# Optimization experiments

Hardware: AMD Instinct MI355X
Metric: run time of the kernel (lower is better)

Reference implementation:

```python
import jax, jax.numpy as jnp
import numpy as np

B, D, U = 4096, 2048, 2048

def hard_sigmoid(x):
    # keras hard_sigmoid: clip(0.2*x + 0.5, 0, 1)
    return jnp.clip(0.2 * x + 0.5, 0.0, 1.0)

def setup_inputs() -> dict:
    key = jax.random.key(0)
    k1, k2, k3, k4, k5 = jax.random.split(key, 5)
    return {
        "inputs": jax.random.normal(k1, (B, D), dtype=jnp.float32),
        "h_tm1": jax.random.normal(k2, (B, U), dtype=jnp.float32),
        "c_tm1": jax.random.normal(k3, (B, U), dtype=jnp.float32),
        "kernel": jax.random.normal(k4, (D, 4 * U), dtype=jnp.float32) * 0.02,
        "recurrent_kernel": jax.random.normal(k5, (U, 4 * U), dtype=jnp.float32) * 0.02,
    }

def reference(inputs, h_tm1, c_tm1, kernel, recurrent_kernel):
    u = kernel.shape[1] // 4
    # One fused GEMM each for input and recurrent paths (same math as 8 split GEMMs)
    z = inputs @ kernel + h_tm1 @ recurrent_kernel  # [B, 4U]
    z_i, z_f, z_c, z_o = jnp.split(z, 4, axis=1)
    i = hard_sigmoid(z_i)
    f = hard_sigmoid(z_f)
    c = f * c_tm1 + i * jnp.tanh(z_c)
    o = hard_sigmoid(z_o)
    h = o * jnp.tanh(c)
    return (h, h, c)
```

## Files before the change

### kernel.cpp

```cpp
#include <hip/hip_runtime.h>
#include <stdint.h>

typedef unsigned short u16;
typedef float f32x4 __attribute__((ext_vector_type(4)));
typedef __bf16 bf16x8 __attribute__((ext_vector_type(8)));

#define B_ 4096
#define D_ 2048
#define U_ 2048
#define K_ 4096
#define N_ 8192
#define NIT 32

__device__ __forceinline__ u16 f32_bf16(float f) {
  uint32_t u = __float_as_uint(f);
  u += 0x7FFFu + ((u >> 16) & 1u);
  return (u16)(u >> 16);
}
__device__ __forceinline__ float hsig(float x) {
  return fminf(fmaxf(0.2f * x + 0.5f, 0.0f), 1.0f);
}
__device__ __forceinline__ float ftanh(float x) {
  x = fminf(fmaxf(x, -15.0f), 15.0f);
  float e = __expf(2.0f * x);
  return (e - 1.0f) / (e + 1.0f);
}
__device__ __forceinline__ void gload16(const void* g, void* l) {
  __builtin_amdgcn_global_load_lds(
      (const __attribute__((address_space(1))) void*)g,
      (__attribute__((address_space(3))) void*)l,
      16, 0, 0);
}

__global__ __launch_bounds__(256) void cast_a(const float* __restrict__ x,
                                              const float* __restrict__ h,
                                              u16* __restrict__ A) {
  int c = blockIdx.x * 256 + threadIdx.x;
  int m = c >> 9;
  int kc = (c & 511) << 3;
  const float* src = (kc < D_) ? (x + (size_t)m * D_ + kc)
                               : (h + (size_t)m * U_ + (kc - D_));
  float4 v0 = ((const float4*)src)[0];
  float4 v1 = ((const float4*)src)[1];
  u16 o[8] = { f32_bf16(v0.x), f32_bf16(v0.y), f32_bf16(v0.z), f32_bf16(v0.w),
               f32_bf16(v1.x), f32_bf16(v1.y), f32_bf16(v1.z), f32_bf16(v1.w) };
  *(uint4*)(A + (size_t)c * 8) = *(const uint4*)o;
}

__global__ __launch_bounds__(256) void cast_wt(const float* __restrict__ kern,
                                               const float* __restrict__ rker,
                                               u16* __restrict__ Wt) {
  __shared__ u16 sW[64][68];
  const int t = threadIdx.x;
  const int bx = blockIdx.x;
  const int by = blockIdx.y;
  const int k0 = by * 64;
  const float* src = (k0 < D_) ? kern : rker;
  const int krow0 = (k0 < D_) ? k0 : (k0 - D_);
#pragma unroll
  for (int i = 0; i < 4; ++i) {
    int c = i * 256 + t;
    int kl = c >> 4;
    int nq = c & 15;
    int g  = nq >> 2;
    int ul = (nq & 3) << 2;
    int n  = g * U_ + bx * 16 + ul;
    float4 v = *(const float4*)(src + (size_t)(krow0 + kl) * N_ + n);
    u16 p[4] = { f32_bf16(v.x), f32_bf16(v.y), f32_bf16(v.z), f32_bf16(v.w) };
    *(ushort4*)&sW[kl][g * 16 + ul] = *(const ushort4*)p;
  }
  __syncthreads();
#pragma unroll
  for (int j = 0; j < 2; ++j) {
    int c2 = j * 256 + t;
    int nl = c2 >> 3;
    int kc = c2 & 7;
    u16 p[8];
#pragma unroll
    for (int jj = 0; jj < 8; ++jj) p[jj] = sW[kc * 8 + jj][nl];
    *(uint4*)(Wt + ((size_t)bx * 64 + nl) * K_ + k0 + kc * 8) = *(const uint4*)p;
  }
}

#define ABASE(par, kk) ((par) * 65536 + (kk) * 16384)
#define BBASE(par, kk) ((par) * 65536 + 32768 + (kk) * 16384)

#define STAGE_A(par, kk, t) do { \
  const u16* gp_ = Ab + (size_t)grow * K_ + (t) * 64 + (kk) * 32 + gch8; \
  char* lp_ = ldsc + ABASE(par, kk) + wid * 1024; \
  gload16(gp_, lp_); \
  gload16(gp_ + (size_t)128 * K_, lp_ + 8192); \
} while (0)

#define STAGE_B(par, kk, t) do { \
  const u16* gp_ = Bb + (size_t)grow * K_ + (t) * 64 + (kk) * 32 + gch8; \
  char* lp_ = ldsc + BBASE(par, kk) + wid * 1024; \
  gload16(gp_, lp_); \
  gload16(gp_ + (size_t)128 * K_, lp_ + 8192); \
} while (0)

#define VMW(n) asm volatile("s_waitcnt vmcnt(" #n ")" ::: "memory")

#define MFMA16(mh) do { \
  _Pragma("unroll") \
  for (int m_ = 0; m_ < 4; ++m_) { \
    _Pragma("unroll") \
    for (int n_ = 0; n_ < 4; ++n_) \
      acc[(mh) * 4 + m_][n_] = __builtin_amdgcn_mfma_f32_16x16x32_bf16( \
          av[m_], bv[n_], acc[(mh) * 4 + m_][n_], 0, 0, 0); \
  } \
} while (0)

#define PHASE(par, kk, mh, RB, STAGE_STMT, TAIL_STMT) do { \
  const char* pab_ = ldsc + ABASE(par, kk); \
  _Pragma("unroll") \
  for (int m_ = 0; m_ < 4; ++m_) \
    av[m_] = *(const bf16x8*)(pab_ + aoff + (mh) * 4096 + m_ * 1024); \
  if (RB) { \
    const char* pbb_ = ldsc + BBASE(par, kk); \
    _Pragma("unroll") \
    for (int n_ = 0; n_ < 4; ++n_) \
      bv[n_] = *(const bf16x8*)(pbb_ + boff + n_ * 1024); \
  } \
  STAGE_STMT; \
  __builtin_amdgcn_s_barrier(); \
  asm volatile("s_waitcnt lgkmcnt(0)" ::: "memory"); \
  __builtin_amdgcn_s_setprio(1); \
  MFMA16(mh); \
  __builtin_amdgcn_s_setprio(0); \
  TAIL_STMT; \
  __builtin_amdgcn_s_barrier(); \
} while (0)

__global__ __launch_bounds__(512, 2) void lstm_gemm(const u16* __restrict__ A,
                                                    const u16* __restrict__ Wt,
                                                    const float* __restrict__ c_prev,
                                                    float* __restrict__ out) {
  __shared__ __align__(16) u16 lds[65536];
  char* ldsc = (char*)lds;
  const int tid  = threadIdx.x;
  const int lane = tid & 63;
  const int wid  = tid >> 6;
  const int wr   = wid >> 2;
  const int wcn  = wid & 3;
  const int fr   = lane & 15;
  const int fq   = lane >> 4;

  const int orig = blockIdx.x;
  const int wg   = ((orig & 7) << 6) | (orig >> 3);
  const int bm   = wg & 15;
  const int bn   = wg >> 4;

  const u16* Ab = A  + (size_t)bm * 256 * K_;
  const u16* Bb = Wt + (size_t)bn * 256 * K_;

  const int grow = tid >> 2;
  const int gch8 = (((tid & 3) ^ ((grow >> 1) & 3)) << 3);
  const int csw  = (fq ^ ((fr >> 1) & 3)) << 4;
  const int aoff = (wr * 128 + fr) * 64 + csw;
  const int boff = (wcn * 64 + fr) * 64 + csw;

  f32x4 acc[8][4] = {};
  bf16x8 av[4], bv[4];

  STAGE_A(0, 0, 0);
  STAGE_B(0, 0, 0);
  STAGE_A(0, 1, 0);
  STAGE_B(0, 1, 0);
  STAGE_A(1, 0, 1);
  STAGE_B(1, 0, 1);
  VMW(4);
  __builtin_amdgcn_s_barrier();

  for (int i = 0; i < NIT; ++i) {
    const int t1 = 2 * i + 1;
    const int t2 = 2 * i + 2;
    const int t3 = 2 * i + 3;
    const bool nl = (i + 1 < NIT);
    PHASE(0, 0, 0, 1, { STAGE_A(1, 1, t1); }, {});
    PHASE(0, 0, 1, 0, { STAGE_B(1, 1, t1); }, {});
    PHASE(0, 1, 0, 1, { if (nl) STAGE_A(0, 0, t2); }, {});
    PHASE(0, 1, 1, 0, { if (nl) STAGE_B(0, 0, t2); },
          { if (nl) { VMW(4); } else { VMW(0); } });
    PHASE(1, 0, 0, 1, { if (nl) STAGE_A(0, 1, t2); }, {});
    PHASE(1, 0, 1, 0, { if (nl) STAGE_B(0, 1, t2); }, {});
    PHASE(1, 1, 0, 1, { if (nl) STAGE_A(1, 0, t3); }, {});
    PHASE(1, 1, 1, 0, { if (nl) STAGE_B(1, 0, t3); }, { VMW(4); });
  }

  const int u  = (bn * 4 + wcn) * 16 + fr;
  const size_t BU = (size_t)B_ * U_;
#pragma unroll
  for (int mi = 0; mi < 8; ++mi) {
#pragma unroll
    for (int r = 0; r < 4; ++r) {
      int row = bm * 256 + wr * 128 + mi * 16 + fq * 4 + r;
      float zi = acc[mi][0][r], zf = acc[mi][1][r];
      float zc = acc[mi][2][r], zo = acc[mi][3][r];
      float iv = hsig(zi), fv = hsig(zf), ov = hsig(zo);
      size_t off = (size_t)row * U_ + u;
      float cp = c_prev[off];
      float cv = fv * cp + iv * ftanh(zc);
      float hv = ov * ftanh(cv);
      out[off]          = hv;
      out[BU + off]     = hv;
      out[2 * BU + off] = cv;
    }
  }
}

extern "C" void kernel_launch(void* const* d_in, const int* in_sizes, int n_in,
                              void* d_out, int out_size, void* d_ws, size_t ws_size,
                              hipStream_t stream) {
  const float* x  = (const float*)d_in[0];
  const float* h  = (const float*)d_in[1];
  const float* cp = (const float*)d_in[2];
  const float* kk = (const float*)d_in[3];
  const float* rk = (const float*)d_in[4];
  float* out = (float*)d_out;

  const size_t bytesA  = (size_t)B_ * K_ * 2;
  const size_t bytesWt = (size_t)N_ * K_ * 2;
  if (ws_size < bytesA + bytesWt) return;

  u16* Aws = (u16*)d_ws;
  u16* Wt  = (u16*)((char*)d_ws + bytesA);

  cast_a<<<(B_ * K_ / 8) / 256, 256, 0, stream>>>(x, h, Aws);
  cast_wt<<<dim3(N_ / 64, K_ / 64), 256, 0, stream>>>(kk, rk, Wt);
  lstm_gemm<<<dim3(512), dim3(512), 0, stream>>>(Aws, Wt, cp, out);
}
```

Baseline: 309.7 us.

## Switch GEMM to 32x32x16 MFMA with 2x4 wave layout and restructured pipeline

Replaces the 16x16x32 MFMA tiling with 32x32x16 instructions on a 4x2 wave grid (64x128 per wave), which cuts LDS fragment reads per MFMA flop. The per-phase pipeline is rewritten to use one barrier per phase, with staging interleaved between A and B and adjusted vmcnt waits. c_prev is prefetched into registers before the main loop. The weight transpose kernel is widened to 128 output columns per block so it matches the new gate interleaving. The cost is more register pressure from the larger accumulator fragments and the prefetched c_prev values, and there is risk in the single-barrier LDS reuse ordering.

```diff
diff --git a/kernel.cpp b/kernel.cpp
--- a/kernel.cpp
+++ b/kernel.cpp
@@ -2,7 +2,7 @@
 #include <stdint.h>
 
 typedef unsigned short u16;
-typedef float f32x4 __attribute__((ext_vector_type(4)));
+typedef float f32x16 __attribute__((ext_vector_type(16)));
 typedef __bf16 bf16x8 __attribute__((ext_vector_type(8)));
 
 #define B_ 4096
@@ -50,7 +50,7 @@
 __global__ __launch_bounds__(256) void cast_wt(const float* __restrict__ kern,
                                                const float* __restrict__ rker,
                                                u16* __restrict__ Wt) {
-  __shared__ u16 sW[64][68];
+  __shared__ u16 sW[64][134];
   const int t = threadIdx.x;
   const int bx = blockIdx.x;
   const int by = blockIdx.y;
@@ -58,27 +58,26 @@
   const float* src = (k0 < D_) ? kern : rker;
   const int krow0 = (k0 < D_) ? k0 : (k0 - D_);
 #pragma unroll
-  for (int i = 0; i < 4; ++i) {
-    int c = i * 256 + t;
-    int kl = c >> 4;
-    int nq = c & 15;
-    int g  = nq >> 2;
-    int ul = (nq & 3) << 2;
-    int n  = g * U_ + bx * 16 + ul;
+  for (int i = 0; i < 8; ++i) {
+    int q  = i * 256 + t;
+    int kl = q >> 5;
+    int cc = q & 31;
+    int g  = cc >> 3;
+    int n  = g * U_ + bx * 32 + (cc & 7) * 4;
     float4 v = *(const float4*)(src + (size_t)(krow0 + kl) * N_ + n);
     u16 p[4] = { f32_bf16(v.x), f32_bf16(v.y), f32_bf16(v.z), f32_bf16(v.w) };
-    *(ushort4*)&sW[kl][g * 16 + ul] = *(const ushort4*)p;
+    *(ushort4*)&sW[kl][cc * 4] = *(const ushort4*)p;
   }
   __syncthreads();
 #pragma unroll
-  for (int j = 0; j < 2; ++j) {
+  for (int j = 0; j < 4; ++j) {
     int c2 = j * 256 + t;
-    int nl = c2 >> 3;
+    int r  = c2 >> 3;
     int kc = c2 & 7;
     u16 p[8];
 #pragma unroll
-    for (int jj = 0; jj < 8; ++jj) p[jj] = sW[kc * 8 + jj][nl];
-    *(uint4*)(Wt + ((size_t)bx * 64 + nl) * K_ + k0 + kc * 8) = *(const uint4*)p;
+    for (int jj = 0; jj < 8; ++jj) p[jj] = sW[kc * 8 + jj][r];
+    *(uint4*)(Wt + ((size_t)bx * 128 + r) * K_ + k0 + kc * 8) = *(const uint4*)p;
   }
 }
 
@@ -100,36 +99,32 @@
 } while (0)
 
 #define VMW(n) asm volatile("s_waitcnt vmcnt(" #n ")" ::: "memory")
-
-#define MFMA16(mh) do { \
-  _Pragma("unroll") \
-  for (int m_ = 0; m_ < 4; ++m_) { \
-    _Pragma("unroll") \
-    for (int n_ = 0; n_ < 4; ++n_) \
-      acc[(mh) * 4 + m_][n_] = __builtin_amdgcn_mfma_f32_16x16x32_bf16( \
-          av[m_], bv[n_], acc[(mh) * 4 + m_][n_], 0, 0, 0); \
-  } \
-} while (0)
-
-#define PHASE(par, kk, mh, RB, STAGE_STMT, TAIL_STMT) do { \
-  const char* pab_ = ldsc + ABASE(par, kk); \
-  _Pragma("unroll") \
-  for (int m_ = 0; m_ < 4; ++m_) \
-    av[m_] = *(const bf16x8*)(pab_ + aoff + (mh) * 4096 + m_ * 1024); \
-  if (RB) { \
-    const char* pbb_ = ldsc + BBASE(par, kk); \
-    _Pragma("unroll") \
-    for (int n_ = 0; n_ < 4; ++n_) \
-      bv[n_] = *(const bf16x8*)(pbb_ + boff + n_ * 1024); \
-  } \
+#define MFMA32 __builtin_amdgcn_mfma_f32_32x32x16_bf16
+
+#define PHASE(par, kk, ks, STAGE_STMT, VMW_STMT) do { \
+  const char* pa_ = ldsc + ABASE(par, kk) + aob; \
+  const char* pb_ = ldsc + BBASE(par, kk) + bob; \
+  const int ck_ = (ks) ? ck1 : ck0; \
+  bf16x8 av0 = *(const bf16x8*)(pa_ + ck_); \
+  bf16x8 av1 = *(const bf16x8*)(pa_ + 2048 + ck_); \
+  bf16x8 bv0 = *(const bf16x8*)(pb_ + ck_); \
+  bf16x8 bv1 = *(const bf16x8*)(pb_ + 2048 + ck_); \
+  bf16x8 bv2 = *(const bf16x8*)(pb_ + 4096 + ck_); \
+  bf16x8 bv3 = *(const bf16x8*)(pb_ + 6144 + ck_); \
   STAGE_STMT; \
+  VMW_STMT; \
   __builtin_amdgcn_s_barrier(); \
   asm volatile("s_waitcnt lgkmcnt(0)" ::: "memory"); \
   __builtin_amdgcn_s_setprio(1); \
-  MFMA16(mh); \
+  acc[0][0] = MFMA32(av0, bv0, acc[0][0], 0, 0, 0); \
+  acc[0][1] = MFMA32(av0, bv1, acc[0][1], 0, 0, 0); \
+  acc[0][2] = MFMA32(av0, bv2, acc[0][2], 0, 0, 0); \
+  acc[0][3] = MFMA32(av0, bv3, acc[0][3], 0, 0, 0); \
+  acc[1][0] = MFMA32(av1, bv0, acc[1][0], 0, 0, 0); \
+  acc[1][1] = MFMA32(av1, bv1, acc[1][1], 0, 0, 0); \
+  acc[1][2] = MFMA32(av1, bv2, acc[1][2], 0, 0, 0); \
+  acc[1][3] = MFMA32(av1, bv3, acc[1][3], 0, 0, 0); \
   __builtin_amdgcn_s_setprio(0); \
-  TAIL_STMT; \
-  __builtin_amdgcn_s_barrier(); \
 } while (0)
 
 __global__ __launch_bounds__(512, 2) void lstm_gemm(const u16* __restrict__ A,
@@ -141,10 +136,10 @@
   const int tid  = threadIdx.x;
   const int lane = tid & 63;
   const int wid  = tid >> 6;
-  const int wr   = wid >> 2;
-  const int wcn  = wid & 3;
-  const int fr   = lane & 15;
-  const int fq   = lane >> 4;
+  const int wr   = wid >> 1;
+  const int wcn  = wid & 1;
+  const int la   = lane & 31;
+  const int cq   = lane >> 5;
 
   const int orig = blockIdx.x;
   const int wg   = ((orig & 7) << 6) | (orig >> 3);
@@ -156,19 +151,30 @@
 
   const int grow = tid >> 2;
   const int gch8 = (((tid & 3) ^ ((grow >> 1) & 3)) << 3);
-  const int csw  = (fq ^ ((fr >> 1) & 3)) << 4;
-  const int aoff = (wr * 128 + fr) * 64 + csw;
-  const int boff = (wcn * 64 + fr) * 64 + csw;
-
-  f32x4 acc[8][4] = {};
-  bf16x8 av[4], bv[4];
+  const int sw  = (la >> 1) & 3;
+  const int ck0 = ((cq ^ sw)) << 4;
+  const int ck1 = (((2 + cq) ^ sw)) << 4;
+  const int aob = (wr * 64 + la) * 64;
+  const int bob = (wcn * 128 + la) * 64;
+
+  f32x16 acc[2][4] = {};
+
+  const int u  = (bn * 2 + wcn) * 32 + la;
+  const int rowb = bm * 256 + wr * 64 + 4 * cq;
+  float cpv[2][16];
+#pragma unroll
+  for (int rt = 0; rt < 2; ++rt)
+#pragma unroll
+    for (int r = 0; r < 16; ++r) {
+      int row = rowb + rt * 32 + (r & 3) + 8 * (r >> 2);
+      cpv[rt][r] = c_prev[(size_t)row * U_ + u];
+    }
 
   STAGE_A(0, 0, 0);
   STAGE_B(0, 0, 0);
   STAGE_A(0, 1, 0);
   STAGE_B(0, 1, 0);
   STAGE_A(1, 0, 1);
-  STAGE_B(1, 0, 1);
   VMW(4);
   __builtin_amdgcn_s_barrier();
 
@@ -177,30 +183,29 @@
     const int t2 = 2 * i + 2;
     const int t3 = 2 * i + 3;
     const bool nl = (i + 1 < NIT);
-    PHASE(0, 0, 0, 1, { STAGE_A(1, 1, t1); }, {});
-    PHASE(0, 0, 1, 0, { STAGE_B(1, 1, t1); }, {});
-    PHASE(0, 1, 0, 1, { if (nl) STAGE_A(0, 0, t2); }, {});
-    PHASE(0, 1, 1, 0, { if (nl) STAGE_B(0, 0, t2); },
-          { if (nl) { VMW(4); } else { VMW(0); } });
-    PHASE(1, 0, 0, 1, { if (nl) STAGE_A(0, 1, t2); }, {});
-    PHASE(1, 0, 1, 0, { if (nl) STAGE_B(0, 1, t2); }, {});
-    PHASE(1, 1, 0, 1, { if (nl) STAGE_A(1, 0, t3); }, {});
-    PHASE(1, 1, 1, 0, { if (nl) STAGE_B(1, 0, t3); }, { VMW(4); });
-  }
-
-  const int u  = (bn * 4 + wcn) * 16 + fr;
+    PHASE(0, 0, 0, { STAGE_B(1, 0, t1); }, {});
+    PHASE(0, 0, 1, { STAGE_A(1, 1, t1); }, { VMW(6); });
+    PHASE(0, 1, 0, { STAGE_B(1, 1, t1); }, {});
+    PHASE(0, 1, 1, { if (nl) STAGE_A(0, 0, t2); },
+          { if (nl) { VMW(6); } else { VMW(4); } });
+    PHASE(1, 0, 0, { if (nl) STAGE_B(0, 0, t2); }, {});
+    PHASE(1, 0, 1, { if (nl) STAGE_A(0, 1, t2); },
+          { if (nl) { VMW(6); } else { VMW(0); } });
+    PHASE(1, 1, 0, { if (nl) STAGE_B(0, 1, t2); }, {});
+    PHASE(1, 1, 1, { if (nl) STAGE_A(1, 0, t3); }, { if (nl) { VMW(6); } });
+  }
+
   const size_t BU = (size_t)B_ * U_;
 #pragma unroll
-  for (int mi = 0; mi < 8; ++mi) {
-#pragma unroll
-    for (int r = 0; r < 4; ++r) {
-      int row = bm * 256 + wr * 128 + mi * 16 + fq * 4 + r;
-      float zi = acc[mi][0][r], zf = acc[mi][1][r];
-      float zc = acc[mi][2][r], zo = acc[mi][3][r];
+  for (int rt = 0; rt < 2; ++rt) {
+#pragma unroll
+    for (int r = 0; r < 16; ++r) {
+      int row = rowb + rt * 32 + (r & 3) + 8 * (r >> 2);
+      float zi = acc[rt][0][r], zf = acc[rt][1][r];
+      float zc = acc[rt][2][r], zo = acc[rt][3][r];
       float iv = hsig(zi), fv = hsig(zf), ov = hsig(zo);
       size_t off = (size_t)row * U_ + u;
-      float cp = c_prev[off];
-      float cv = fv * cp + iv * ftanh(zc);
+      float cv = fv * cpv[rt][r] + iv * ftanh(zc);
       float hv = ov * ftanh(cv);
       out[off]          = hv;
       out[BU + off]     = hv;
@@ -227,6 +232,6 @@
   u16* Wt  = (u16*)((char*)d_ws + bytesA);
 
   cast_a<<<(B_ * K_ / 8) / 256, 256, 0, stream>>>(x, h, Aws);
-  cast_wt<<<dim3(N_ / 64, K_ / 64), 256, 0, stream>>>(kk, rk, Wt);
+  cast_wt<<<dim3(64, 64), 256, 0, stream>>>(kk, rk, Wt);
   lstm_gemm<<<dim3(512), dim3(512), 0, stream>>>(Aws, Wt, cp, out);
 }
```

Result: no change. 315.5 us (+1.9%).

## Shrink GEMM tile to 256x128 with triple-buffered 32-wide K stages

Applied to the files above, without the earlier changes.

Halves the N tile per workgroup (256x128 instead of 256x256) and doubles the grid to 1024 blocks. K is now staged in 32-element slices through a three-slot LDS ring of about 72KB, replacing the previous 128KB double buffer. Launch bounds move to 4 blocks per SM so more workgroups can be resident and hide latency. The cost is lower arithmetic intensity per tile, more A-tile reloads across N, and more barriers per K step.

```diff
diff --git a/kernel.cpp b/kernel.cpp
--- a/kernel.cpp
+++ b/kernel.cpp
@@ -10,7 +10,7 @@
 #define U_ 2048
 #define K_ 4096
 #define N_ 8192
-#define NIT 32
+#define NT 128
 
 __device__ __forceinline__ u16 f32_bf16(float f) {
   uint32_t u = __float_as_uint(f);
@@ -82,119 +82,105 @@
   }
 }
 
-#define ABASE(par, kk) ((par) * 65536 + (kk) * 16384)
-#define BBASE(par, kk) ((par) * 65536 + 32768 + (kk) * 16384)
-
-#define STAGE_A(par, kk, t) do { \
-  const u16* gp_ = Ab + (size_t)grow * K_ + (t) * 64 + (kk) * 32 + gch8; \
-  char* lp_ = ldsc + ABASE(par, kk) + wid * 1024; \
-  gload16(gp_, lp_); \
-  gload16(gp_ + (size_t)128 * K_, lp_ + 8192); \
+#define LDSA(par) ((par) * 24576)
+#define LDSB(par) ((par) * 24576 + 16384)
+
+#define STAGE3(par, t) do { \
+  const u16* ga_ = Ab + (size_t)grow * K_ + (t) * 32 + gch8; \
+  char* la_ = ldsc + LDSA(par) + wid * 1024; \
+  gload16(ga_, la_); \
+  gload16(ga_ + (size_t)128 * K_, la_ + 8192); \
+  gload16(Bb + (size_t)grow * K_ + (t) * 32 + gch8, \
+          ldsc + LDSB(par) + wid * 1024); \
 } while (0)
 
-#define STAGE_B(par, kk, t) do { \
-  const u16* gp_ = Bb + (size_t)grow * K_ + (t) * 64 + (kk) * 32 + gch8; \
-  char* lp_ = ldsc + BBASE(par, kk) + wid * 1024; \
-  gload16(gp_, lp_); \
-  gload16(gp_ + (size_t)128 * K_, lp_ + 8192); \
-} while (0)
-
 #define VMW(n) asm volatile("s_waitcnt vmcnt(" #n ")" ::: "memory")
-
-#define MFMA16(mh) do { \
-  _Pragma("unroll") \
-  for (int m_ = 0; m_ < 4; ++m_) { \
-    _Pragma("unroll") \
-    for (int n_ = 0; n_ < 4; ++n_) \
-      acc[(mh) * 4 + m_][n_] = __builtin_amdgcn_mfma_f32_16x16x32_bf16( \
-          av[m_], bv[n_], acc[(mh) * 4 + m_][n_], 0, 0, 0); \
-  } \
-} while (0)
-
-#define PHASE(par, kk, mh, RB, STAGE_STMT, TAIL_STMT) do { \
-  const char* pab_ = ldsc + ABASE(par, kk); \
-  _Pragma("unroll") \
-  for (int m_ = 0; m_ < 4; ++m_) \
-    av[m_] = *(const bf16x8*)(pab_ + aoff + (mh) * 4096 + m_ * 1024); \
+#define MFMA16 __builtin_amdgcn_mfma_f32_16x16x32_bf16
+
+#define PHASE(par, mh, RB, STAGE_STMT, VMW_STMT) do { \
+  const char* pa_ = ldsc + LDSA(par) + aob + (mh) * 2048; \
+  av0 = *(const bf16x8*)(pa_); \
+  av1 = *(const bf16x8*)(pa_ + 1024); \
   if (RB) { \
-    const char* pbb_ = ldsc + BBASE(par, kk); \
-    _Pragma("unroll") \
-    for (int n_ = 0; n_ < 4; ++n_) \
-      bv[n_] = *(const bf16x8*)(pbb_ + boff + n_ * 1024); \
+    const char* pb_ = ldsc + LDSB(par) + bob; \
+    bv0 = *(const bf16x8*)(pb_); \
+    bv1 = *(const bf16x8*)(pb_ + 1024); \
+    bv2 = *(const bf16x8*)(pb_ + 2048); \
+    bv3 = *(const bf16x8*)(pb_ + 3072); \
   } \
   STAGE_STMT; \
+  VMW_STMT; \
   __builtin_amdgcn_s_barrier(); \
   asm volatile("s_waitcnt lgkmcnt(0)" ::: "memory"); \
   __builtin_amdgcn_s_setprio(1); \
-  MFMA16(mh); \
+  acc[(mh) * 2 + 0][0] = MFMA16(av0, bv0, acc[(mh) * 2 + 0][0], 0, 0, 0); \
+  acc[(mh) * 2 + 0][1] = MFMA16(av0, bv1, acc[(mh) * 2 + 0][1], 0, 0, 0); \
+  acc[(mh) * 2 + 0][2] = MFMA16(av0, bv2, acc[(mh) * 2 + 0][2], 0, 0, 0); \
+  acc[(mh) * 2 + 0][3] = MFMA16(av0, bv3, acc[(mh) * 2 + 0][3], 0, 0, 0); \
+  acc[(mh) * 2 + 1][0] = MFMA16(av1, bv0, acc[(mh) * 2 + 1][0], 0, 0, 0); \
+  acc[(mh) * 2 + 1][1] = MFMA16(av1, bv1, acc[(mh) * 2 + 1][1], 0, 0, 0); \
+  acc[(mh) * 2 + 1][2] = MFMA16(av1, bv2, acc[(mh) * 2 + 1][2], 0, 0, 0); \
+  acc[(mh) * 2 + 1][3] = MFMA16(av1, bv3, acc[(mh) * 2 + 1][3], 0, 0, 0); \
   __builtin_amdgcn_s_setprio(0); \
-  TAIL_STMT; \
-  __builtin_amdgcn_s_barrier(); \
 } while (0)
 
-__global__ __launch_bounds__(512, 2) void lstm_gemm(const u16* __restrict__ A,
+__global__ __launch_bounds__(512, 4) void lstm_gemm(const u16* __restrict__ A,
                                                     const u16* __restrict__ Wt,
                                                     const float* __restrict__ c_prev,
                                                     float* __restrict__ out) {
-  __shared__ __align__(16) u16 lds[65536];
+  __shared__ __align__(16) u16 lds[36864];
   char* ldsc = (char*)lds;
   const int tid  = threadIdx.x;
   const int lane = tid & 63;
   const int wid  = tid >> 6;
-  const int wr   = wid >> 2;
-  const int wcn  = wid & 3;
+  const int wr   = wid >> 1;
+  const int wcn  = wid & 1;
   const int fr   = lane & 15;
   const int fq   = lane >> 4;
 
   const int orig = blockIdx.x;
-  const int wg   = ((orig & 7) << 6) | (orig >> 3);
+  const int wg   = ((orig & 7) << 7) | (orig >> 3);
   const int bm   = wg & 15;
   const int bn   = wg >> 4;
 
   const u16* Ab = A  + (size_t)bm * 256 * K_;
-  const u16* Bb = Wt + (size_t)bn * 256 * K_;
+  const u16* Bb = Wt + (size_t)bn * 128 * K_;
 
   const int grow = tid >> 2;
   const int gch8 = (((tid & 3) ^ ((grow >> 1) & 3)) << 3);
-  const int csw  = (fq ^ ((fr >> 1) & 3)) << 4;
-  const int aoff = (wr * 128 + fr) * 64 + csw;
-  const int boff = (wcn * 64 + fr) * 64 + csw;
-
-  f32x4 acc[8][4] = {};
-  bf16x8 av[4], bv[4];
-
-  STAGE_A(0, 0, 0);
-  STAGE_B(0, 0, 0);
-  STAGE_A(0, 1, 0);
-  STAGE_B(0, 1, 0);
-  STAGE_A(1, 0, 1);
-  STAGE_B(1, 0, 1);
-  VMW(4);
+  const int csw = (fq ^ ((fr >> 1) & 3)) << 4;
+  const int aob = (wr * 64 + fr) * 64 + csw;
+  const int bob = (wcn * 64 + fr) * 64 + csw;
+
+  f32x4 acc[4][4] = {};
+  bf16x8 av0, av1, bv0, bv1, bv2, bv3;
+
+  STAGE3(0, 0);
+  STAGE3(1, 1);
+  VMW(3);
   __builtin_amdgcn_s_barrier();
 
-  for (int i = 0; i < NIT; ++i) {
-    const int t1 = 2 * i + 1;
-    const int t2 = 2 * i + 2;
-    const int t3 = 2 * i + 3;
-    const bool nl = (i + 1 < NIT);
-    PHASE(0, 0, 0, 1, { STAGE_A(1, 1, t1); }, {});
-    PHASE(0, 0, 1, 0, { STAGE_B(1, 1, t1); }, {});
-    PHASE(0, 1, 0, 1, { if (nl) STAGE_A(0, 0, t2); }, {});
-    PHASE(0, 1, 1, 0, { if (nl) STAGE_B(0, 0, t2); },
-          { if (nl) { VMW(4); } else { VMW(0); } });
-    PHASE(1, 0, 0, 1, { if (nl) STAGE_A(0, 1, t2); }, {});
-    PHASE(1, 0, 1, 0, { if (nl) STAGE_B(0, 1, t2); }, {});
-    PHASE(1, 1, 0, 1, { if (nl) STAGE_A(1, 0, t3); }, {});
-    PHASE(1, 1, 1, 0, { if (nl) STAGE_B(1, 0, t3); }, { VMW(4); });
-  }
-
-  const int u  = (bn * 4 + wcn) * 16 + fr;
+  for (int tb = 0; tb < NT; tb += 3) {
+    PHASE(0, 0, 1, {}, {});
+    PHASE(0, 1, 0, { if (tb + 2 < NT) STAGE3(2, tb + 2); },
+          { if (tb + 2 < NT) { VMW(3); } else { VMW(0); } });
+    if (tb + 1 >= NT) break;
+    PHASE(1, 0, 1, {}, {});
+    PHASE(1, 1, 0, { if (tb + 3 < NT) STAGE3(0, tb + 3); },
+          { if (tb + 3 < NT) { VMW(3); } else { VMW(0); } });
+    if (tb + 2 >= NT) break;
+    PHASE(2, 0, 1, {}, {});
+    PHASE(2, 1, 0, { if (tb + 4 < NT) STAGE3(1, tb + 4); },
+          { if (tb + 4 < NT) { VMW(3); } else { VMW(0); } });
+  }
+
+  const int u  = (bn * 2 + wcn) * 16 + fr;
   const size_t BU = (size_t)B_ * U_;
 #pragma unroll
-  for (int mi = 0; mi < 8; ++mi) {
+  for (int mi = 0; mi < 4; ++mi) {
 #pragma unroll
     for (int r = 0; r < 4; ++r) {
-      int row = bm * 256 + wr * 128 + mi * 16 + fq * 4 + r;
+      int row = bm * 256 + wr * 64 + mi * 16 + fq * 4 + r;
       float zi = acc[mi][0][r], zf = acc[mi][1][r];
       float zc = acc[mi][2][r], zo = acc[mi][3][r];
       float iv = hsig(zi), fv = hsig(zf), ov = hsig(zo);
@@ -228,5 +214,5 @@
 
   cast_a<<<(B_ * K_ / 8) / 256, 256, 0, stream>>>(x, h, Aws);
   cast_wt<<<dim3(N_ / 64, K_ / 64), 256, 0, stream>>>(kk, rk, Wt);
-  lstm_gemm<<<dim3(512), dim3(512), 0, stream>>>(Aws, Wt, cp, out);
-}
+  lstm_gemm<<<dim3(1024), dim3(512), 0, stream>>>(Aws, Wt, cp, out);
+}
```

New measurement: 1.059 ms. +242.0%, slower.

## Restructure GEMM main loop into 4-stage ring with one barrier per K-step

Applied to the files above, without the earlier changes.

Replaces the 8-phase loop, where each phase covered half the M-fragments and had two barriers, with a 4-slot LDS ring of 32-wide K tiles. Each phase loads all 8 A and 4 B fragments, issues the next stage's global-to-LDS loads, waits with vmcnt, and runs 32 MFMAs behind a single barrier. This halves the barrier count per MFMA and deepens prefetch to about two tiles ahead. The cost is more VGPRs for the A fragments (8 instead of 4). The ring reuses a slot one phase after it was read with no trailing barrier, which risks a race if a fast wave overwrites LDS another wave is still reading.

```diff
diff --git a/kernel.cpp b/kernel.cpp
--- a/kernel.cpp
+++ b/kernel.cpp
@@ -10,7 +10,7 @@
 #define U_ 2048
 #define K_ 4096
 #define N_ 8192
-#define NIT 32
+#define NT_ 128
 
 __device__ __forceinline__ u16 f32_bf16(float f) {
   uint32_t u = __float_as_uint(f);
@@ -82,54 +82,43 @@
   }
 }
 
-#define ABASE(par, kk) ((par) * 65536 + (kk) * 16384)
-#define BBASE(par, kk) ((par) * 65536 + 32768 + (kk) * 16384)
-
-#define STAGE_A(par, kk, t) do { \
-  const u16* gp_ = Ab + (size_t)grow * K_ + (t) * 64 + (kk) * 32 + gch8; \
-  char* lp_ = ldsc + ABASE(par, kk) + wid * 1024; \
-  gload16(gp_, lp_); \
-  gload16(gp_ + (size_t)128 * K_, lp_ + 8192); \
+#define LDSA(par) ((par) * 32768)
+#define LDSB(par) ((par) * 32768 + 16384)
+
+#define STAGE4(par, t) do { \
+  const u16* ga_ = Ab + (size_t)grow * K_ + (t) * 32 + gch8; \
+  const u16* gb_ = Bb + (size_t)grow * K_ + (t) * 32 + gch8; \
+  char* la_ = ldsc + LDSA(par) + wid * 1024; \
+  char* lb_ = ldsc + LDSB(par) + wid * 1024; \
+  gload16(ga_, la_); \
+  gload16(ga_ + (size_t)128 * K_, la_ + 8192); \
+  gload16(gb_, lb_); \
+  gload16(gb_ + (size_t)128 * K_, lb_ + 8192); \
 } while (0)
 
-#define STAGE_B(par, kk, t) do { \
-  const u16* gp_ = Bb + (size_t)grow * K_ + (t) * 64 + (kk) * 32 + gch8; \
-  char* lp_ = ldsc + BBASE(par, kk) + wid * 1024; \
-  gload16(gp_, lp_); \
-  gload16(gp_ + (size_t)128 * K_, lp_ + 8192); \
-} while (0)
-
 #define VMW(n) asm volatile("s_waitcnt vmcnt(" #n ")" ::: "memory")
-
-#define MFMA16(mh) do { \
+#define MFMA16 __builtin_amdgcn_mfma_f32_16x16x32_bf16
+
+#define PHASE(par, STAGE_STMT, VMW_STMT) do { \
+  const char* pa_ = ldsc + LDSA(par) + aob; \
+  const char* pb_ = ldsc + LDSB(par) + bob; \
   _Pragma("unroll") \
-  for (int m_ = 0; m_ < 4; ++m_) { \
+  for (int m_ = 0; m_ < 8; ++m_) av[m_] = *(const bf16x8*)(pa_ + m_ * 1024); \
+  _Pragma("unroll") \
+  for (int n_ = 0; n_ < 4; ++n_) bv[n_] = *(const bf16x8*)(pb_ + n_ * 1024); \
+  STAGE_STMT; \
+  VMW_STMT; \
+  __builtin_amdgcn_s_barrier(); \
+  asm volatile("s_waitcnt lgkmcnt(0)" ::: "memory"); \
+  __builtin_amdgcn_sched_barrier(0); \
+  __builtin_amdgcn_s_setprio(1); \
+  _Pragma("unroll") \
+  for (int m_ = 0; m_ < 8; ++m_) { \
     _Pragma("unroll") \
     for (int n_ = 0; n_ < 4; ++n_) \
-      acc[(mh) * 4 + m_][n_] = __builtin_amdgcn_mfma_f32_16x16x32_bf16( \
-          av[m_], bv[n_], acc[(mh) * 4 + m_][n_], 0, 0, 0); \
+      acc[m_][n_] = MFMA16(av[m_], bv[n_], acc[m_][n_], 0, 0, 0); \
   } \
-} while (0)
-
-#define PHASE(par, kk, mh, RB, STAGE_STMT, TAIL_STMT) do { \
-  const char* pab_ = ldsc + ABASE(par, kk); \
-  _Pragma("unroll") \
-  for (int m_ = 0; m_ < 4; ++m_) \
-    av[m_] = *(const bf16x8*)(pab_ + aoff + (mh) * 4096 + m_ * 1024); \
-  if (RB) { \
-    const char* pbb_ = ldsc + BBASE(par, kk); \
-    _Pragma("unroll") \
-    for (int n_ = 0; n_ < 4; ++n_) \
-      bv[n_] = *(const bf16x8*)(pbb_ + boff + n_ * 1024); \
-  } \
-  STAGE_STMT; \
-  __builtin_amdgcn_s_barrier(); \
-  asm volatile("s_waitcnt lgkmcnt(0)" ::: "memory"); \
-  __builtin_amdgcn_s_setprio(1); \
-  MFMA16(mh); \
   __builtin_amdgcn_s_setprio(0); \
-  TAIL_STMT; \
-  __builtin_amdgcn_s_barrier(); \
 } while (0)
 
 __global__ __launch_bounds__(512, 2) void lstm_gemm(const u16* __restrict__ A,
@@ -156,36 +145,25 @@
 
   const int grow = tid >> 2;
   const int gch8 = (((tid & 3) ^ ((grow >> 1) & 3)) << 3);
-  const int csw  = (fq ^ ((fr >> 1) & 3)) << 4;
-  const int aoff = (wr * 128 + fr) * 64 + csw;
-  const int boff = (wcn * 64 + fr) * 64 + csw;
+  const int csw = (fq ^ ((fr >> 1) & 3)) << 4;
+  const int aob = (wr * 128 + fr) * 64 + csw;
+  const int bob = (wcn * 64 + fr) * 64 + csw;
 
   f32x4 acc[8][4] = {};
-  bf16x8 av[4], bv[4];
-
-  STAGE_A(0, 0, 0);
-  STAGE_B(0, 0, 0);
-  STAGE_A(0, 1, 0);
-  STAGE_B(0, 1, 0);
-  STAGE_A(1, 0, 1);
-  STAGE_B(1, 0, 1);
+  bf16x8 av[8], bv[4];
+
+  STAGE4(0, 0);
+  STAGE4(1, 1);
   VMW(4);
   __builtin_amdgcn_s_barrier();
 
-  for (int i = 0; i < NIT; ++i) {
-    const int t1 = 2 * i + 1;
-    const int t2 = 2 * i + 2;
-    const int t3 = 2 * i + 3;
-    const bool nl = (i + 1 < NIT);
-    PHASE(0, 0, 0, 1, { STAGE_A(1, 1, t1); }, {});
-    PHASE(0, 0, 1, 0, { STAGE_B(1, 1, t1); }, {});
-    PHASE(0, 1, 0, 1, { if (nl) STAGE_A(0, 0, t2); }, {});
-    PHASE(0, 1, 1, 0, { if (nl) STAGE_B(0, 0, t2); },
-          { if (nl) { VMW(4); } else { VMW(0); } });
-    PHASE(1, 0, 0, 1, { if (nl) STAGE_A(0, 1, t2); }, {});
-    PHASE(1, 0, 1, 0, { if (nl) STAGE_B(0, 1, t2); }, {});
-    PHASE(1, 1, 0, 1, { if (nl) STAGE_A(1, 0, t3); }, {});
-    PHASE(1, 1, 1, 0, { if (nl) STAGE_B(1, 0, t3); }, { VMW(4); });
+  for (int tb = 0; tb < NT_; tb += 4) {
+    PHASE(0, { STAGE4(2, tb + 2); }, { VMW(4); });
+    PHASE(1, { STAGE4(3, tb + 3); }, { VMW(4); });
+    PHASE(2, { if (tb + 4 < NT_) STAGE4(0, tb + 4); },
+          { if (tb + 4 < NT_) { VMW(4); } else { VMW(0); } });
+    PHASE(3, { if (tb + 5 < NT_) STAGE4(1, tb + 5); },
+          { if (tb + 5 < NT_) { VMW(4); } });
   }
 
   const int u  = (bn * 4 + wcn) * 16 + fr;
```

New measurement: 305.7 us. About the same (-1.3%).
